# Kernel tuning notes

Hardware: AMD Instinct MI355X
Metric: run time of the kernel (lower is better)

Reference implementation:

```python
import jax, jax.numpy as jnp
import numpy as np

N_NODES = 50000
N_EDGES = 400000
NUM_FEATS = 128
LATENT_DIM_Y = 64
HIDDEN = 512
OUT = 2


def gcn_conv(x, edge_index, W, b, num_nodes):
    """PyG GCNConv: add self-loops, symmetric normalization, x @ W then scatter-add."""
    x = x @ W  # [N, out_ch]
    loop = jnp.arange(num_nodes)
    row = jnp.concatenate([edge_index[0], loop])  # source nodes
    col = jnp.concatenate([edge_index[1], loop])  # target nodes
    deg = jax.ops.segment_sum(jnp.ones_like(col, dtype=x.dtype), col, num_segments=num_nodes)
    dinv = jnp.where(deg > 0, jax.lax.rsqrt(deg), 0.0)
    norm = dinv[row] * dinv[col]  # [E+N]
    msgs = norm[:, None] * x[row]  # gather source features, scale
    out = jax.ops.segment_sum(msgs, col, num_segments=num_nodes)
    return out + b


def setup_inputs() -> dict:
    key = jax.random.key(0)
    k1, k2, k3, k4, k5, k6, k7 = jax.random.split(key, 7)
    in_ch = NUM_FEATS + LATENT_DIM_Y
    inputs = {
        "edge_index": jax.random.randint(k1, (2, N_EDGES), 0, N_NODES),
        "X": jax.random.normal(k2, (N_NODES, NUM_FEATS), dtype=jnp.float32),
        "u_Y": jax.random.normal(k3, (N_NODES, LATENT_DIM_Y), dtype=jnp.float32),
        "W1": jax.random.normal(k4, (in_ch, HIDDEN), dtype=jnp.float32) / np.sqrt(in_ch),
        "b1": jnp.zeros((HIDDEN,), dtype=jnp.float32),
        "W2": jax.random.normal(k5, (HIDDEN, OUT), dtype=jnp.float32) / np.sqrt(HIDDEN),
        "b2": jnp.zeros((OUT,), dtype=jnp.float32),
    }
    return inputs


def reference(edge_index, X, u_Y, W1, b1, W2, b2):
    latent = jnp.concatenate([u_Y, X], axis=1)  # [N, latent+feats]
    h = jax.nn.relu(gcn_conv(latent, edge_index, W1, b1, N_NODES))
    y = gcn_conv(h, edge_index, W2, b2, N_NODES)
    # nn.Softmax() on a 2D tensor defaults to dim=1
    return jax.nn.softmax(y, axis=1)
```

## Files before the change

kernel.cpp:

```cpp
#include <hip/hip_runtime.h>

#define N_NODES 50000
#define N_EDGES 400000
#define FEATS   128
#define LAT     64
#define IN_CH   192
#define HID     512
#define MB      64
#define NB      196
#define CAP     64

#define E4       100000
#define SC_BLKS  391
#define CVT_BLKS 9375
#define W1_BLKS  384

typedef __attribute__((ext_vector_type(8))) short bf16x8;
typedef __attribute__((ext_vector_type(4))) float f32x4;

static inline int cdiv(int a, int b) { return (a + b - 1) / b; }

__device__ __forceinline__ unsigned short f2bf(float f) {
    unsigned int u = __float_as_uint(f);
    u = (u + 0x7fffu + ((u >> 16) & 1u)) >> 16;
    return (unsigned short)u;
}
__device__ __forceinline__ float bf_lo(unsigned int u) {
    return __uint_as_float(u << 16);
}
__device__ __forceinline__ float bf_hi(unsigned int u) {
    return __uint_as_float(u & 0xffff0000u);
}

__global__ __launch_bounds__(256) void
k_front(const int* __restrict__ ei, int* __restrict__ cursor, int* __restrict__ csr_src,
        const float* __restrict__ uY, const float* __restrict__ X,
        unsigned short* __restrict__ latent,
        const float* __restrict__ W1, unsigned short* __restrict__ W1f) {
    int bid = blockIdx.x;
    if (bid < SC_BLKS) {
        int i4 = bid * 256 + threadIdx.x;
        if (i4 < E4) {
            int4 r = ((const int4*)ei)[i4];
            int4 c = ((const int4*)(ei + N_EDGES))[i4];
            int p0 = atomicAdd(&cursor[c.x], 1);
            int p1 = atomicAdd(&cursor[c.y], 1);
            int p2 = atomicAdd(&cursor[c.z], 1);
            int p3 = atomicAdd(&cursor[c.w], 1);
            csr_src[c.x * CAP + p0] = r.x;
            csr_src[c.y * CAP + p1] = r.y;
            csr_src[c.z * CAP + p2] = r.z;
            csr_src[c.w * CAP + p3] = r.w;
        }
    } else if (bid < SC_BLKS + CVT_BLKS) {
        int idx = (bid - SC_BLKS) * 256 + threadIdx.x;
        int i = idx / 48, q = idx % 48;
        const float4* uY4 = (const float4*)uY;
        const float4* X4  = (const float4*)X;
        float4 v = (q < LAT / 4) ? uY4[i * (LAT / 4) + q]
                                 : X4[i * (FEATS / 4) + (q - LAT / 4)];
        uint2 o;
        o.x = (unsigned int)f2bf(v.x) | ((unsigned int)f2bf(v.y) << 16);
        o.y = (unsigned int)f2bf(v.z) | ((unsigned int)f2bf(v.w) << 16);
        ((uint2*)latent)[idx] = o;
    } else {
        int idx = (bid - SC_BLKS - CVT_BLKS) * 256 + threadIdx.x;
        if (idx < IN_CH * HID) {
            int k = idx / HID, n = idx % HID;
            int ntile = n >> 4, nn = n & 15;
            int kc = k >> 5, q = (k >> 3) & 3, j = k & 7;
            int dst = (((ntile * 6 + kc) * 64 + q * 16 + nn) << 3) + j;
            W1f[dst] = f2bf(W1[idx]);
        }
    }
}

__global__ __launch_bounds__(256) void
k_dinv(const int* __restrict__ cursor, float* __restrict__ dinv) {
    int i = blockIdx.x * 256 + threadIdx.x;
    if (i < N_NODES) dinv[i] = rsqrtf((float)(cursor[i] + 1));
}

__global__ __launch_bounds__(256) void
k_gather_agg(const int* __restrict__ cursor, const int* __restrict__ csr_src,
             const float* __restrict__ dinv,
             const unsigned short* __restrict__ latent, unsigned short* __restrict__ agg) {
    int w    = blockIdx.x * 4 + (threadIdx.x >> 6);
    int lane = threadIdx.x & 63;
    if (w >= N_NODES) return;
    int qt = lane >> 4, l = lane & 15;
    int c0 = l * 6;
    const unsigned int* __restrict__ L = (const unsigned int*)latent;

    float di = dinv[w];
    float acc[12];
    if (qt == 0) {
        const unsigned int* p = L + w * 96 + c0;
#pragma unroll
        for (int d = 0; d < 6; ++d) {
            unsigned int u = p[d];
            acc[2 * d]     = di * bf_lo(u);
            acc[2 * d + 1] = di * bf_hi(u);
        }
    } else {
#pragma unroll
        for (int d = 0; d < 12; ++d) acc[d] = 0.f;
    }

    int jlo = w * CAP, jhi = jlo + cursor[w];
    int j = jlo + qt;
    int r = (j < jhi) ? csr_src[j] : 0;
    for (; j < jhi; j += 4) {
        int rn = (j + 4 < jhi) ? csr_src[j + 4] : 0;
        float wt = dinv[r];
        const unsigned int* p = L + r * 96 + c0;
        unsigned int u0 = p[0], u1 = p[1], u2 = p[2], u3 = p[3], u4 = p[4], u5 = p[5];
        acc[0]  = fmaf(wt, bf_lo(u0), acc[0]);
        acc[1]  = fmaf(wt, bf_hi(u0), acc[1]);
        acc[2]  = fmaf(wt, bf_lo(u1), acc[2]);
        acc[3]  = fmaf(wt, bf_hi(u1), acc[3]);
        acc[4]  = fmaf(wt, bf_lo(u2), acc[4]);
        acc[5]  = fmaf(wt, bf_hi(u2), acc[5]);
        acc[6]  = fmaf(wt, bf_lo(u3), acc[6]);
        acc[7]  = fmaf(wt, bf_hi(u3), acc[7]);
        acc[8]  = fmaf(wt, bf_lo(u4), acc[8]);
        acc[9]  = fmaf(wt, bf_hi(u4), acc[9]);
        acc[10] = fmaf(wt, bf_lo(u5), acc[10]);
        acc[11] = fmaf(wt, bf_hi(u5), acc[11]);
        r = rn;
    }

#pragma unroll
    for (int d = 0; d < 12; ++d) {
        acc[d] += __shfl_xor(acc[d], 16);
        acc[d] += __shfl_xor(acc[d], 32);
    }

    if (qt == 0) {
        unsigned int* qp = (unsigned int*)agg + w * 96 + c0;
#pragma unroll
        for (int d = 0; d < 6; ++d)
            qp[d] = (unsigned int)f2bf(di * acc[2 * d]) |
                    ((unsigned int)f2bf(di * acc[2 * d + 1]) << 16);
    }
}

__global__ __launch_bounds__(256, 2) void
k_gemm_mfma(const unsigned short* __restrict__ agg, const unsigned short* __restrict__ W1f,
            const float* __restrict__ b1, const float* __restrict__ W2,
            float* __restrict__ y_pre) {
    __shared__ unsigned short Af[MB * IN_CH];
    __shared__ float red[4][MB][2];

    int t  = threadIdx.x;
    int m0 = blockIdx.x * MB;

    {
        const uint4* src = (const uint4*)agg;
        for (int idx = t; idx < MB * 24; idx += 256) {
            int row = idx / 24, c = idx % 24;
            int g = m0 + row;
            uint4 v = make_uint4(0u, 0u, 0u, 0u);
            if (g < N_NODES) v = src[(size_t)g * 24 + c];
            int mt = row >> 4, m = row & 15, kc = c >> 2, q = c & 3;
            ((uint4*)Af)[(mt * 6 + kc) * 64 + q * 16 + m] = v;
        }
    }
    __syncthreads();

    int wid = t >> 6, lane = t & 63;
    int nl = lane & 15, q = lane >> 4;

    float b1v[8], w2a[8], w2b[8];
#pragma unroll
    for (int nt = 0; nt < 8; ++nt) {
        int n = wid * 128 + nt * 16 + nl;
        b1v[nt] = b1[n];
        w2a[nt] = W2[n * 2 + 0];
        w2b[nt] = W2[n * 2 + 1];
    }

    f32x4 acc[4][8];
#pragma unroll
    for (int mt = 0; mt < 4; ++mt)
#pragma unroll
        for (int nt = 0; nt < 8; ++nt) acc[mt][nt] = (f32x4){0.f, 0.f, 0.f, 0.f};

    const bf16x8* Afv = (const bf16x8*)Af;
    const bf16x8* Bv  = (const bf16x8*)W1f;
#pragma unroll
    for (int kc = 0; kc < 6; ++kc) {
        bf16x8 a[4];
#pragma unroll
        for (int mt = 0; mt < 4; ++mt) a[mt] = Afv[(mt * 6 + kc) * 64 + lane];
#pragma unroll
        for (int nt = 0; nt < 8; ++nt) {
            bf16x8 b = Bv[((wid * 8 + nt) * 6 + kc) * 64 + lane];
#pragma unroll
            for (int mt = 0; mt < 4; ++mt)
                acc[mt][nt] = __builtin_amdgcn_mfma_f32_16x16x32_bf16(a[mt], b, acc[mt][nt], 0, 0, 0);
        }
    }

#pragma unroll
    for (int mt = 0; mt < 4; ++mt) {
#pragma unroll
        for (int r = 0; r < 4; ++r) {
            float p0 = 0.f, p1 = 0.f;
#pragma unroll
            for (int nt = 0; nt < 8; ++nt) {
                float h = fmaxf(acc[mt][nt][r] + b1v[nt], 0.f);
                p0 = fmaf(h, w2a[nt], p0);
                p1 = fmaf(h, w2b[nt], p1);
            }
#pragma unroll
            for (int off = 1; off < 16; off <<= 1) {
                p0 += __shfl_xor(p0, off);
                p1 += __shfl_xor(p1, off);
            }
            if (nl == 0) {
                int row = mt * 16 + q * 4 + r;
                red[wid][row][0] = p0;
                red[wid][row][1] = p1;
            }
        }
    }
    __syncthreads();
    if (t < MB * 2) {
        int row = t >> 1, j = t & 1;
        float s = red[0][row][j] + red[1][row][j] + red[2][row][j] + red[3][row][j];
        int g = m0 + row;
        if (g < N_NODES) y_pre[g * 2 + j] = s;
    }
}

__global__ __launch_bounds__(256) void
k_gather_y(const int* __restrict__ cursor, const int* __restrict__ csr_src,
           const float* __restrict__ dinv,
           const float* __restrict__ y_pre, const float* __restrict__ b2,
           float* __restrict__ out) {
    int i  = blockIdx.x * 32 + (threadIdx.x >> 3);
    int l8 = threadIdx.x & 7;
    if (i >= N_NODES) return;
    const float2* __restrict__ yp = (const float2*)y_pre;
    float di = dinv[i];
    float a0 = 0.f, a1 = 0.f;
    if (l8 == 0) {
        float2 v = yp[i];
        a0 = di * v.x;
        a1 = di * v.y;
    }
    int jlo = i * CAP, jhi = jlo + cursor[i];
    for (int j = jlo + l8; j < jhi; j += 8) {
        int   r  = csr_src[j];
        float wt = dinv[r];
        float2 v = yp[r];
        a0 = fmaf(wt, v.x, a0);
        a1 = fmaf(wt, v.y, a1);
    }
#pragma unroll
    for (int off = 1; off < 8; off <<= 1) {
        a0 += __shfl_xor(a0, off);
        a1 += __shfl_xor(a1, off);
    }
    if (l8 == 0) {
        float ya = di * a0 + b2[0];
        float yb = di * a1 + b2[1];
        float mx = fmaxf(ya, yb);
        float e0 = expf(ya - mx);
        float e1 = expf(yb - mx);
        float inv = 1.0f / (e0 + e1);
        out[i * 2 + 0] = e0 * inv;
        out[i * 2 + 1] = e1 * inv;
    }
}


extern "C" void kernel_launch(void* const* d_in, const int* in_sizes, int n_in,
                              void* d_out, int out_size, void* d_ws, size_t ws_size,
                              hipStream_t stream) {
    const int*   ei = (const int*)d_in[0];
    const float* X  = (const float*)d_in[1];
    const float* uY = (const float*)d_in[2];
    const float* W1 = (const float*)d_in[3];
    const float* b1 = (const float*)d_in[4];
    const float* W2 = (const float*)d_in[5];
    const float* b2 = (const float*)d_in[6];
    float* out = (float*)d_out;

    char* ws = (char*)d_ws;
    auto carve = [&](size_t bytes) {
        char* p = ws;
        ws += (bytes + 255) & ~size_t(255);
        return p;
    };
    int*   cursor    = (int*)carve(N_NODES * sizeof(int));
    int*   csr_src   = (int*)carve((size_t)N_NODES * CAP * sizeof(int));
    float* dinv      = (float*)carve(N_NODES * sizeof(float));
    unsigned short* latent = (unsigned short*)carve((size_t)N_NODES * IN_CH * 2);
    unsigned short* aggb   = (unsigned short*)carve((size_t)N_NODES * IN_CH * 2);
    unsigned short* W1f    = (unsigned short*)carve((size_t)IN_CH * HID * 2);
    float* y_pre     = (float*)carve((size_t)N_NODES * 2 * sizeof(float));

    hipMemsetAsync(cursor, 0, N_NODES * sizeof(int), stream);

    k_front     <<<SC_BLKS + CVT_BLKS + W1_BLKS, 256, 0, stream>>>(
                      ei, cursor, csr_src, uY, X, latent, W1, W1f);
    k_dinv      <<<NB, 256, 0, stream>>>(cursor, dinv);

    k_gather_agg<<<cdiv(N_NODES, 4), 256, 0, stream>>>(
                      cursor, csr_src, dinv, latent, aggb);

    k_gemm_mfma <<<cdiv(N_NODES, MB), 256, 0, stream>>>(aggb, W1f, b1, W2, y_pre);

    k_gather_y  <<<cdiv(N_NODES, 32), 256, 0, stream>>>(
                      cursor, csr_src, dinv, y_pre, b2, out);
}
```

Before: 179.6 us.

## Drop dinv kernel, compute rsqrt inline, vectorize gather with 8-lane edge groups

Removes the separate dinv kernel and its buffer, recomputing degree normalization inline from cursor in both gather kernels. The layer-1 gather now uses 8 edge groups of 8 lanes, each lane loading three uint4 per row instead of six dwords, and issues the first two neighbor rows before the loop to expose memory parallelism. CAP shrinks from 64 to 32, halving the CSR footprint but assuming no node exceeds 32 in-edges, which is a risk with random graphs. Unconditional loads at slots qt+7 may read stale entries, which are clamped and given zero weight.

Measured after the change: 186.9 us. +4.1%, slower.

```diff
diff --git a/kernel.cpp b/kernel.cpp
--- a/kernel.cpp
+++ b/kernel.cpp
@@ -7,8 +7,7 @@
 #define IN_CH   192
 #define HID     512
 #define MB      64
-#define NB      196
-#define CAP     64
+#define CAP     32
 
 #define E4       100000
 #define SC_BLKS  391
@@ -75,73 +74,95 @@
     }
 }
 
-__global__ __launch_bounds__(256) void
-k_dinv(const int* __restrict__ cursor, float* __restrict__ dinv) {
-    int i = blockIdx.x * 256 + threadIdx.x;
-    if (i < N_NODES) dinv[i] = rsqrtf((float)(cursor[i] + 1));
+__device__ __forceinline__ void load_row(uint4* a, const uint4* __restrict__ L4,
+                                         int r, int l8) {
+    const uint4* p = L4 + (size_t)r * 24 + l8 * 3;
+    a[0] = p[0]; a[1] = p[1]; a[2] = p[2];
+}
+__device__ __forceinline__ void fma_row(float* acc, const uint4* a, float wt) {
+#pragma unroll
+    for (int i = 0; i < 3; ++i) {
+        unsigned int u0 = a[i].x, u1 = a[i].y, u2 = a[i].z, u3 = a[i].w;
+        acc[i * 8 + 0] = fmaf(wt, bf_lo(u0), acc[i * 8 + 0]);
+        acc[i * 8 + 1] = fmaf(wt, bf_hi(u0), acc[i * 8 + 1]);
+        acc[i * 8 + 2] = fmaf(wt, bf_lo(u1), acc[i * 8 + 2]);
+        acc[i * 8 + 3] = fmaf(wt, bf_hi(u1), acc[i * 8 + 3]);
+        acc[i * 8 + 4] = fmaf(wt, bf_lo(u2), acc[i * 8 + 4]);
+        acc[i * 8 + 5] = fmaf(wt, bf_hi(u2), acc[i * 8 + 5]);
+        acc[i * 8 + 6] = fmaf(wt, bf_lo(u3), acc[i * 8 + 6]);
+        acc[i * 8 + 7] = fmaf(wt, bf_hi(u3), acc[i * 8 + 7]);
+    }
 }
 
 __global__ __launch_bounds__(256) void
 k_gather_agg(const int* __restrict__ cursor, const int* __restrict__ csr_src,
-             const float* __restrict__ dinv,
              const unsigned short* __restrict__ latent, unsigned short* __restrict__ agg) {
     int w    = blockIdx.x * 4 + (threadIdx.x >> 6);
     int lane = threadIdx.x & 63;
     if (w >= N_NODES) return;
-    int qt = lane >> 4, l = lane & 15;
-    int c0 = l * 6;
-    const unsigned int* __restrict__ L = (const unsigned int*)latent;
-
-    float di = dinv[w];
-    float acc[12];
+    int qt = lane >> 3, l8 = lane & 7;
+    const uint4* __restrict__ L4 = (const uint4*)latent;
+
+    int jlo = w * CAP;
+    int deg  = cursor[w];
+    int rawe = csr_src[jlo + max(qt - 1, 0)];
+    int raw2 = csr_src[jlo + qt + 7];
+    int raw1 = (qt == 0) ? w : rawe;
+    int r1 = min(max(raw1, 0), N_NODES - 1);
+    int r2 = min(max(raw2, 0), N_NODES - 1);
+    int d1 = cursor[r1];
+    int d2 = cursor[r2];
+
+    uint4 a[3];
+    load_row(a, L4, r1, l8);
+
+    float di = rsqrtf((float)(deg + 1));
+    float w1 = (qt == 0) ? di
+             : ((qt - 1 < deg) ? rsqrtf((float)(d1 + 1)) : 0.f);
+
+    float acc[24];
+#pragma unroll
+    for (int i = 0; i < 24; ++i) acc[i] = 0.f;
+
+    bool more = (deg > 7);
+    uint4 b[3];
+    if (more) load_row(b, L4, r2, l8);
+
+    fma_row(acc, a, w1);
+    if (more) {
+        float w2 = (qt + 7 < deg) ? rsqrtf((float)(d2 + 1)) : 0.f;
+        fma_row(acc, b, w2);
+        for (int e = 15 + qt; e < deg; e += 8) {
+            int r = csr_src[jlo + e];
+            float wt = rsqrtf((float)(cursor[r] + 1));
+            uint4 t[3];
+            load_row(t, L4, r, l8);
+            fma_row(acc, t, wt);
+        }
+    }
+
+#pragma unroll
+    for (int i = 0; i < 24; ++i) {
+        acc[i] += __shfl_xor(acc[i], 8);
+        acc[i] += __shfl_xor(acc[i], 16);
+        acc[i] += __shfl_xor(acc[i], 32);
+    }
+
     if (qt == 0) {
-        const unsigned int* p = L + w * 96 + c0;
-#pragma unroll
-        for (int d = 0; d < 6; ++d) {
-            unsigned int u = p[d];
-            acc[2 * d]     = di * bf_lo(u);
-            acc[2 * d + 1] = di * bf_hi(u);
-        }
-    } else {
-#pragma unroll
-        for (int d = 0; d < 12; ++d) acc[d] = 0.f;
-    }
-
-    int jlo = w * CAP, jhi = jlo + cursor[w];
-    int j = jlo + qt;
-    int r = (j < jhi) ? csr_src[j] : 0;
-    for (; j < jhi; j += 4) {
-        int rn = (j + 4 < jhi) ? csr_src[j + 4] : 0;
-        float wt = dinv[r];
-        const unsigned int* p = L + r * 96 + c0;
-        unsigned int u0 = p[0], u1 = p[1], u2 = p[2], u3 = p[3], u4 = p[4], u5 = p[5];
-        acc[0]  = fmaf(wt, bf_lo(u0), acc[0]);
-        acc[1]  = fmaf(wt, bf_hi(u0), acc[1]);
-        acc[2]  = fmaf(wt, bf_lo(u1), acc[2]);
-        acc[3]  = fmaf(wt, bf_hi(u1), acc[3]);
-        acc[4]  = fmaf(wt, bf_lo(u2), acc[4]);
-        acc[5]  = fmaf(wt, bf_hi(u2), acc[5]);
-        acc[6]  = fmaf(wt, bf_lo(u3), acc[6]);
-        acc[7]  = fmaf(wt, bf_hi(u3), acc[7]);
-        acc[8]  = fmaf(wt, bf_lo(u4), acc[8]);
-        acc[9]  = fmaf(wt, bf_hi(u4), acc[9]);
-        acc[10] = fmaf(wt, bf_lo(u5), acc[10]);
-        acc[11] = fmaf(wt, bf_hi(u5), acc[11]);
-        r = rn;
-    }
-
-#pragma unroll
-    for (int d = 0; d < 12; ++d) {
-        acc[d] += __shfl_xor(acc[d], 16);
-        acc[d] += __shfl_xor(acc[d], 32);
-    }
-
-    if (qt == 0) {
-        unsigned int* qp = (unsigned int*)agg + w * 96 + c0;
-#pragma unroll
-        for (int d = 0; d < 6; ++d)
-            qp[d] = (unsigned int)f2bf(di * acc[2 * d]) |
-                    ((unsigned int)f2bf(di * acc[2 * d + 1]) << 16);
+        uint4* op = (uint4*)agg + (size_t)w * 24 + l8 * 3;
+#pragma unroll
+        for (int v = 0; v < 3; ++v) {
+            uint4 o;
+            o.x = (unsigned int)f2bf(di * acc[v * 8 + 0]) |
+                  ((unsigned int)f2bf(di * acc[v * 8 + 1]) << 16);
+            o.y = (unsigned int)f2bf(di * acc[v * 8 + 2]) |
+                  ((unsigned int)f2bf(di * acc[v * 8 + 3]) << 16);
+            o.z = (unsigned int)f2bf(di * acc[v * 8 + 4]) |
+                  ((unsigned int)f2bf(di * acc[v * 8 + 5]) << 16);
+            o.w = (unsigned int)f2bf(di * acc[v * 8 + 6]) |
+                  ((unsigned int)f2bf(di * acc[v * 8 + 7]) << 16);
+            op[v] = o;
+        }
     }
 }
 
@@ -236,27 +257,39 @@
 
 __global__ __launch_bounds__(256) void
 k_gather_y(const int* __restrict__ cursor, const int* __restrict__ csr_src,
-           const float* __restrict__ dinv,
            const float* __restrict__ y_pre, const float* __restrict__ b2,
            float* __restrict__ out) {
     int i  = blockIdx.x * 32 + (threadIdx.x >> 3);
     int l8 = threadIdx.x & 7;
     if (i >= N_NODES) return;
     const float2* __restrict__ yp = (const float2*)y_pre;
-    float di = dinv[i];
-    float a0 = 0.f, a1 = 0.f;
-    if (l8 == 0) {
-        float2 v = yp[i];
-        a0 = di * v.x;
-        a1 = di * v.y;
-    }
-    int jlo = i * CAP, jhi = jlo + cursor[i];
-    for (int j = jlo + l8; j < jhi; j += 8) {
-        int   r  = csr_src[j];
-        float wt = dinv[r];
-        float2 v = yp[r];
-        a0 = fmaf(wt, v.x, a0);
-        a1 = fmaf(wt, v.y, a1);
+
+    int jlo = i * CAP;
+    int deg  = cursor[i];
+    int rawe = csr_src[jlo + max(l8 - 1, 0)];
+    int raw2 = csr_src[jlo + l8 + 7];
+    int raw1 = (l8 == 0) ? i : rawe;
+    int r1 = min(max(raw1, 0), N_NODES - 1);
+    int r2 = min(max(raw2, 0), N_NODES - 1);
+    int d1 = cursor[r1], d2 = cursor[r2];
+    float2 v1 = yp[r1];
+
+    float di = rsqrtf((float)(deg + 1));
+    float w1 = (l8 == 0) ? di
+             : ((l8 - 1 < deg) ? rsqrtf((float)(d1 + 1)) : 0.f);
+    float a0 = w1 * v1.x, a1 = w1 * v1.y;
+    if (deg > 7) {
+        float2 v2 = yp[r2];
+        float w2 = (l8 + 7 < deg) ? rsqrtf((float)(d2 + 1)) : 0.f;
+        a0 = fmaf(w2, v2.x, a0);
+        a1 = fmaf(w2, v2.y, a1);
+        for (int e = 15 + l8; e < deg; e += 8) {
+            int r = csr_src[jlo + e];
+            float wt = rsqrtf((float)(cursor[r] + 1));
+            float2 v = yp[r];
+            a0 = fmaf(wt, v.x, a0);
+            a1 = fmaf(wt, v.y, a1);
+        }
     }
 #pragma unroll
     for (int off = 1; off < 8; off <<= 1) {
@@ -296,7 +329,6 @@
     };
     int*   cursor    = (int*)carve(N_NODES * sizeof(int));
     int*   csr_src   = (int*)carve((size_t)N_NODES * CAP * sizeof(int));
-    float* dinv      = (float*)carve(N_NODES * sizeof(float));
     unsigned short* latent = (unsigned short*)carve((size_t)N_NODES * IN_CH * 2);
     unsigned short* aggb   = (unsigned short*)carve((size_t)N_NODES * IN_CH * 2);
     unsigned short* W1f    = (unsigned short*)carve((size_t)IN_CH * HID * 2);
@@ -306,13 +338,12 @@
 
     k_front     <<<SC_BLKS + CVT_BLKS + W1_BLKS, 256, 0, stream>>>(
                       ei, cursor, csr_src, uY, X, latent, W1, W1f);
-    k_dinv      <<<NB, 256, 0, stream>>>(cursor, dinv);
 
     k_gather_agg<<<cdiv(N_NODES, 4), 256, 0, stream>>>(
-                      cursor, csr_src, dinv, latent, aggb);
+                      cursor, csr_src, latent, aggb);
 
     k_gemm_mfma <<<cdiv(N_NODES, MB), 256, 0, stream>>>(aggb, W1f, b1, W2, y_pre);
 
     k_gather_y  <<<cdiv(N_NODES, 32), 256, 0, stream>>>(
-                      cursor, csr_src, dinv, y_pre, b2, out);
-}
+                      cursor, csr_src, y_pre, b2, out);
+}
```
